# Kernel tuning notes

Measured on AMD Instinct MI355X. Metric: run time of the kernel, lower is better.

The kernel has to match this reference:

```python
import jax, jax.numpy as jnp
import numpy as np

DIM = 64
K = 7
GC = 8            # groups_channels (hardcoded in module)
G = DIM // GC     # groups = 8
RED = 2           # reduction_ratio
PAD = (K - 1) // 2


def _patches(y, k, p):
    # torch nn.Unfold(k, dilation=1, padding=p, stride=1) ordering: (c, kh, kw)
    b, c, H, W = y.shape
    yp = jnp.pad(y, ((0, 0), (0, 0), (p, p), (p, p)))
    tiles = [yp[:, :, i:i + H, j:j + W] for i in range(k) for j in range(k)]
    return jnp.stack(tiles, axis=2)  # (b, c, k*k, H, W)


def setup_inputs() -> dict:
    key = jax.random.key(0)
    ks = jax.random.split(key, 6)
    b, h, w = 4, 128, 128
    input_x = jax.random.normal(ks[0], (b, DIM, h, w), dtype=jnp.float32)
    input_y = jax.random.normal(ks[1], (b, DIM, h, w), dtype=jnp.float32)
    c_mid = DIM // RED
    w1 = jax.random.normal(ks[2], (c_mid, DIM), dtype=jnp.float32) * 0.05
    b1 = jnp.zeros((c_mid,), dtype=jnp.float32)
    w2 = jax.random.normal(ks[3], (K * K * G, c_mid), dtype=jnp.float32) * 0.05
    b2 = jnp.zeros((K * K * G,), dtype=jnp.float32)
    return {"input_x": input_x, "input_y": input_y, "w1": w1, "b1": b1, "w2": w2, "b2": b2}


def reference(input_x, input_y, w1, b1, w2, b2):
    b, c, h, w = input_x.shape
    # 1x1 convs generating dynamic kernels (stride == 1, no avgpool)
    mid = jnp.einsum('bchw,oc->bohw', input_x, w1) + b1[None, :, None, None]
    weight = jnp.einsum('bchw,oc->bohw', mid, w2) + b2[None, :, None, None]
    # (b, G, 1, k*k, h, w) broadcast over groups_channels
    weight = weight.reshape(b, G, K * K, h, w)[:, :, None]
    # unfold input_y -> (b, G, GC, k*k, h, w)
    out = _patches(input_y, K, PAD).reshape(b, G, GC, K * K, h, w)
    out = (weight * out).sum(axis=3).reshape(b, DIM, h, w)
    return out
```

## Files before the change

### kernel.cpp

```cpp
#include <hip/hip_runtime.h>
#include <hip/hip_fp16.h>

#define DIMC 64
#define KS 7
#define NTAP 49
#define GCH 8
#define NG 8
#define CMID 32
#define PADD 3
#define HH 128
#define WW 128
#define PLANE (HH*WW)
#define TW 32
#define TH 8
#define TPX (TW+2*PADD)
#define TPY (TH+2*PADD)
#define NPIX (TPX*TPY)
#define NB 4
#define WTSTR 36
#define CPAD 12

#define WC_OFF 0
#define BC_OFF 65536
#define WS_NEED ((size_t)BC_OFF + 2048)

typedef __attribute__((ext_vector_type(8))) short short8;
typedef __attribute__((ext_vector_type(4))) float f32x4;
typedef __fp16 fp16x2 __attribute__((ext_vector_type(2)));

static __device__ inline unsigned short f2bs(float f) {
    union { float f; unsigned u; } v; v.f = f;
    unsigned r = v.u + 0x7fff + ((v.u >> 16) & 1);
    return (unsigned short)(r >> 16);
}

static __device__ inline unsigned pkh(float a, float b) {
    union { fp16x2 h; unsigned u; } c;
    c.h = __builtin_amdgcn_cvt_pkrtz(a, b);
    return c.u;
}

__global__ __launch_bounds__(256)
void prep_wc(const float* __restrict__ w1, const float* __restrict__ b1,
             const float* __restrict__ w2, const float* __restrict__ b2,
             unsigned short* __restrict__ wc, float* __restrict__ bc) {
    const int idx = blockIdx.x * 256 + threadIdx.x;
    const int row64 = idx >> 4;
    const int c0 = (idx & 15) * 4;
    const int g = row64 >> 6, r = row64 & 63;
    float a0 = 0.f, a1 = 0.f, a2 = 0.f, a3 = 0.f, bv = 0.f;
    if (r < NTAP) {
        const float* w2r = w2 + (g * NTAP + r) * CMID;
        #pragma unroll
        for (int m = 0; m < CMID; ++m) {
            float wv = w2r[m];
            const float* w1r = w1 + m * DIMC + c0;
            a0 = fmaf(wv, w1r[0], a0);
            a1 = fmaf(wv, w1r[1], a1);
            a2 = fmaf(wv, w1r[2], a2);
            a3 = fmaf(wv, w1r[3], a3);
        }
        if (c0 == 0) {
            bv = b2[g * NTAP + r];
            #pragma unroll
            for (int m = 0; m < CMID; ++m) bv = fmaf(w2r[m], b1[m], bv);
        }
    }
    *reinterpret_cast<uint2*>(wc + row64 * DIMC + c0) =
        make_uint2(((unsigned)f2bs(a1) << 16) | f2bs(a0),
                   ((unsigned)f2bs(a3) << 16) | f2bs(a2));
    if ((idx & 15) == 0) bc[row64] = bv;
}

__global__ __launch_bounds__(256, 4)
void invol_mfma9_kernel(const float* __restrict__ x, const float* __restrict__ y,
                        const unsigned short* __restrict__ wc,
                        const float* __restrict__ bc,
                        float* __restrict__ out) {
    __shared__ __half ytile[NPIX * GCH];
    __shared__ __half wtl[256 * WTSTR];

    const int tid = threadIdx.x;
    const int l = tid & 63, w = tid >> 6;
    const int fr = l & 15, fk = l >> 4;
    const int bx = blockIdx.x, by = blockIdx.y;
    const int b = blockIdx.z >> 3, g = blockIdx.z & 7;
    const int tx = tid & 31, ty = tid >> 5;

    int gpix[4];
    #pragma unroll
    for (int nt = 0; nt < 4; ++nt) {
        int lp = w * 64 + nt * 16 + fr;
        gpix[nt] = (by * TH + (lp >> 5)) * WW + bx * TW + (lp & 31);
    }

    const float* xb = x + (size_t)b * DIMC * PLANE;
    short8 bf[2][4];
    #pragma unroll
    for (int kp = 0; kp < 2; ++kp)
        #pragma unroll
        for (int nt = 0; nt < 4; ++nt) {
            const float* xp = xb + (size_t)(kp * 32 + fk * 8) * PLANE + gpix[nt];
            unsigned d[4];
            #pragma unroll
            for (int jj = 0; jj < 4; ++jj) {
                float v0 = xp[(size_t)(2 * jj) * PLANE];
                float v1 = xp[(size_t)(2 * jj + 1) * PLANE];
                d[jj] = ((unsigned)f2bs(v1) << 16) | f2bs(v0);
            }
            union { uint4 u; short8 s; } cv;
            cv.u = make_uint4(d[0], d[1], d[2], d[3]);
            bf[kp][nt] = cv.s;
        }

    short8 af[4][2];
    #pragma unroll
    for (int dmt = 0; dmt < 4; ++dmt)
        #pragma unroll
        for (int kp = 0; kp < 2; ++kp) {
            union { uint4 u; short8 s; } cv;
            cv.u = *reinterpret_cast<const uint4*>(
                wc + ((size_t)(g * 64 + dmt * 16 + fr)) * DIMC + kp * 32 + fk * 8);
            af[dmt][kp] = cv.s;
        }

    const float* yg = y + (size_t)(b * DIMC + g * GCH) * PLANE;
    #pragma unroll
    for (int k = 0; k < 5; ++k) {
        int i = tid + k * 256;
        if (i < NPIX * 2) {
            int q  = i / NPIX;
            int px = i - q * NPIX;
            int r = px / TPX, col = px - r * TPX;
            int sy = by * TH + r - PADD, sx = bx * TW + col - PADD;
            bool ok = (sy >= 0 && sy < HH && sx >= 0 && sx < WW);
            const float* yp = yg + (size_t)(q * 4) * PLANE + sy * WW + sx;
            float v0 = ok ? yp[0] : 0.f;
            float v1 = ok ? yp[PLANE] : 0.f;
            float v2 = ok ? yp[2 * PLANE] : 0.f;
            float v3 = ok ? yp[3 * PLANE] : 0.f;
            *reinterpret_cast<uint2*>(&ytile[px * GCH + q * 4]) =
                make_uint2(pkh(v0, v1), pkh(v2, v3));
        }
    }

    __syncthreads();

    __half2 acch[4];
    #pragma unroll
    for (int cc = 0; cc < 4; ++cc) acch[cc] = __float2half2_rn(0.f);
    const int ybase = (ty * TPX + tx) * GCH;

    #pragma unroll
    for (int mc = 0; mc < 2; ++mc) {
        f32x4 acc[2][4];
        #pragma unroll
        for (int dm = 0; dm < 2; ++dm)
            #pragma unroll
            for (int nt = 0; nt < 4; ++nt)
                acc[dm][nt] = f32x4{0.f, 0.f, 0.f, 0.f};

        #pragma unroll
        for (int dm = 0; dm < 2; ++dm)
            #pragma unroll
            for (int kp = 0; kp < 2; ++kp)
                #pragma unroll
                for (int nt = 0; nt < 4; ++nt)
                    acc[dm][nt] = __builtin_amdgcn_mfma_f32_16x16x32_bf16(
                        af[mc * 2 + dm][kp], bf[kp][nt], acc[dm][nt], 0, 0, 0);

        #pragma unroll
        for (int dm = 0; dm < 2; ++dm) {
            int rb = (mc * 2 + dm) * 16 + fk * 4;
            float4 bb = *reinterpret_cast<const float4*>(&bc[g * 64 + rb]);
            #pragma unroll
            for (int nt = 0; nt < 4; ++nt) {
                int lp = w * 64 + nt * 16 + fr;
                *reinterpret_cast<uint2*>(&wtl[lp * WTSTR + dm * 16 + fk * 4]) =
                    make_uint2(pkh(acc[dm][nt][0] + bb.x, acc[dm][nt][1] + bb.y),
                               pkh(acc[dm][nt][2] + bb.z, acc[dm][nt][3] + bb.w));
            }
        }

        uint2 wr[8];
        #pragma unroll
        for (int q = 0; q < 8; ++q)
            wr[q] = *reinterpret_cast<const uint2*>(&wtl[tid * WTSTR + q * 4]);

        const int ninv = (mc == 0) ? 32 : 17;
        #pragma unroll
        for (int j = 0; j < 32; ++j) {
            if (j >= ninv) break;
            const int kk = mc * 32 + j;
            const int ky = kk / 7, kx = kk - ky * 7;
            unsigned uh = (j & 2) ? wr[j >> 2].y : wr[j >> 2].x;
            union { unsigned u; __half2 h; } hc; hc.u = uh;
            __half wh = (j & 1) ? __high2half(hc.h) : __low2half(hc.h);
            __half2 wv2 = __half2half2(wh);
            union { uint4 u; __half2 h[4]; } yvv;
            yvv.u = *reinterpret_cast<const uint4*>(&ytile[ybase + (ky * TPX + kx) * GCH]);
            acch[0] = __hfma2(wv2, yvv.h[0], acch[0]);
            acch[1] = __hfma2(wv2, yvv.h[1], acch[1]);
            acch[2] = __hfma2(wv2, yvv.h[2], acch[2]);
            acch[3] = __hfma2(wv2, yvv.h[3], acch[3]);
        }
    }

    const int gy = by * TH + ty, gx = bx * TW + tx;
    float* op = out + ((size_t)(b * DIMC + g * GCH) * HH + gy) * WW + gx;
    #pragma unroll
    for (int cc = 0; cc < 4; ++cc) {
        float2 f = __half22float2(acch[cc]);
        op[(2 * cc) * PLANE]     = f.x;
        op[(2 * cc + 1) * PLANE] = f.y;
    }
}

__global__ __launch_bounds__(256, 1)
void invol_fused_kernel(const float* __restrict__ x, const float* __restrict__ y,
                        const float* __restrict__ w1, const float* __restrict__ b1,
                        const float* __restrict__ w2, const float* __restrict__ b2,
                        float* __restrict__ out) {
    __shared__ float ytile[NPIX * CPAD];
    const int tid = threadIdx.x;
    const int tx = tid & 31, ty = tid >> 5;
    const int bx = blockIdx.x, by = blockIdx.y, bz = blockIdx.z;
    const int gx = bx * TW + tx, gy = by * TH + ty;

    float xv[DIMC];
    const float* xp = x + ((size_t)(bz * DIMC) * HH + gy) * WW + gx;
    #pragma unroll
    for (int c = 0; c < DIMC; ++c) xv[c] = xp[c * PLANE];

    float mid[CMID];
    #pragma unroll
    for (int m = 0; m < CMID; ++m) {
        float a = b1[m];
        const float4* w1r = reinterpret_cast<const float4*>(w1 + m * DIMC);
        #pragma unroll
        for (int cq = 0; cq < DIMC / 4; ++cq) {
            float4 wv = w1r[cq];
            a = fmaf(wv.x, xv[4*cq+0], a);
            a = fmaf(wv.y, xv[4*cq+1], a);
            a = fmaf(wv.z, xv[4*cq+2], a);
            a = fmaf(wv.w, xv[4*cq+3], a);
        }
        mid[m] = a;
    }

    for (int g = 0; g < NG; ++g) {
        __syncthreads();
        for (int i = tid; i < NPIX * GCH; i += 256) {
            int c = i / NPIX;
            int p = i - c * NPIX;
            int r = p / TPX;
            int col = p - r * TPX;
            int sy = by * TH + r - PADD;
            int sx = bx * TW + col - PADD;
            float v = 0.f;
            if (sy >= 0 && sy < HH && sx >= 0 && sx < WW)
                v = y[((size_t)(bz * DIMC + g * GCH + c) * HH + sy) * WW + sx];
            ytile[p * CPAD + c] = v;
        }
        __syncthreads();

        float wt[NTAP];
        const float*  b2g = b2 + g * NTAP;
        const float4* w2g = reinterpret_cast<const float4*>(w2 + g * NTAP * CMID);
        #pragma unroll
        for (int kk = 0; kk < NTAP; ++kk) {
            float a = b2g[kk];
            #pragma unroll
            for (int mq = 0; mq < CMID / 4; ++mq) {
                float4 wv = w2g[kk * (CMID / 4) + mq];
                a = fmaf(wv.x, mid[4*mq+0], a);
                a = fmaf(wv.y, mid[4*mq+1], a);
                a = fmaf(wv.z, mid[4*mq+2], a);
                a = fmaf(wv.w, mid[4*mq+3], a);
            }
            wt[kk] = a;
        }

        float acc[GCH];
        #pragma unroll
        for (int cc = 0; cc < GCH; ++cc) acc[cc] = 0.f;
        #pragma unroll
        for (int ky = 0; ky < KS; ++ky) {
            #pragma unroll
            for (int kx = 0; kx < KS; ++kx) {
                float wv = wt[ky * KS + kx];
                int pp = (ty + ky) * TPX + (tx + kx);
                const float4* yr = reinterpret_cast<const float4*>(&ytile[pp * CPAD]);
                float4 ya = yr[0];
                float4 yb = yr[1];
                acc[0] = fmaf(wv, ya.x, acc[0]);
                acc[1] = fmaf(wv, ya.y, acc[1]);
                acc[2] = fmaf(wv, ya.z, acc[2]);
                acc[3] = fmaf(wv, ya.w, acc[3]);
                acc[4] = fmaf(wv, yb.x, acc[4]);
                acc[5] = fmaf(wv, yb.y, acc[5]);
                acc[6] = fmaf(wv, yb.z, acc[6]);
                acc[7] = fmaf(wv, yb.w, acc[7]);
            }
        }

        float* op = out + ((size_t)(bz * DIMC + g * GCH) * HH + gy) * WW + gx;
        #pragma unroll
        for (int cc = 0; cc < GCH; ++cc) op[cc * PLANE] = acc[cc];
    }
}

extern "C" void kernel_launch(void* const* d_in, const int* in_sizes, int n_in,
                              void* d_out, int out_size, void* d_ws, size_t ws_size,
                              hipStream_t stream) {
    const float* x  = (const float*)d_in[0];
    const float* y  = (const float*)d_in[1];
    const float* w1 = (const float*)d_in[2];
    const float* b1 = (const float*)d_in[3];
    const float* w2 = (const float*)d_in[4];
    const float* b2 = (const float*)d_in[5];
    float* out = (float*)d_out;

    if (ws_size >= WS_NEED) {
        char* ws = (char*)d_ws;
        unsigned short* wcp = (unsigned short*)(ws + WC_OFF);
        float*          bcp = (float*)(ws + BC_OFF);

        hipLaunchKernelGGL(prep_wc, dim3(32), dim3(256), 0, stream,
                           w1, b1, w2, b2, wcp, bcp);
        hipLaunchKernelGGL(invol_mfma9_kernel, dim3(WW / TW, HH / TH, NB * NG), dim3(256), 0, stream,
                           x, y, wcp, bcp, out);
    } else {
        dim3 grid(WW / TW, HH / TH, NB);
        hipLaunchKernelGGL(invol_fused_kernel, grid, dim3(256), 0, stream,
                           x, y, w1, b1, w2, b2, out);
    }
}
```

Measured before the change: 36.55 us.

## Pre-convert x to channel-interleaved bf16 layout in prep kernel

Adds a pre-pass inside the prep kernel that converts x into a bf16 layout with 8 channels per pixel packed contiguously, stored in workspace. The main kernel then loads each MFMA B fragment with one 16-byte vector load instead of 8 strided fp32 loads plus conversions. Before this, each of the 8 group blocks per batch re-read and re-converted all of x, so the conversion is now done once. The cost is an extra 8 MB workspace write and read, and a larger workspace requirement that could trigger the fallback path if the workspace is too small.

After: 34.54 us. 5.5% less time.

```diff
diff --git a/kernel.cpp b/kernel.cpp
--- a/kernel.cpp
+++ b/kernel.cpp
@@ -22,7 +22,8 @@
 
 #define WC_OFF 0
 #define BC_OFF 65536
-#define WS_NEED ((size_t)BC_OFF + 2048)
+#define XT_OFF 67584
+#define WS_NEED ((size_t)XT_OFF + 8388608)
 
 typedef __attribute__((ext_vector_type(8))) short short8;
 typedef __attribute__((ext_vector_type(4))) float f32x4;
@@ -41,42 +42,65 @@
 }
 
 __global__ __launch_bounds__(256)
-void prep_wc(const float* __restrict__ w1, const float* __restrict__ b1,
-             const float* __restrict__ w2, const float* __restrict__ b2,
-             unsigned short* __restrict__ wc, float* __restrict__ bc) {
-    const int idx = blockIdx.x * 256 + threadIdx.x;
-    const int row64 = idx >> 4;
-    const int c0 = (idx & 15) * 4;
-    const int g = row64 >> 6, r = row64 & 63;
-    float a0 = 0.f, a1 = 0.f, a2 = 0.f, a3 = 0.f, bv = 0.f;
-    if (r < NTAP) {
-        const float* w2r = w2 + (g * NTAP + r) * CMID;
-        #pragma unroll
-        for (int m = 0; m < CMID; ++m) {
-            float wv = w2r[m];
-            const float* w1r = w1 + m * DIMC + c0;
-            a0 = fmaf(wv, w1r[0], a0);
-            a1 = fmaf(wv, w1r[1], a1);
-            a2 = fmaf(wv, w1r[2], a2);
-            a3 = fmaf(wv, w1r[3], a3);
-        }
-        if (c0 == 0) {
-            bv = b2[g * NTAP + r];
-            #pragma unroll
-            for (int m = 0; m < CMID; ++m) bv = fmaf(w2r[m], b1[m], bv);
-        }
-    }
-    *reinterpret_cast<uint2*>(wc + row64 * DIMC + c0) =
-        make_uint2(((unsigned)f2bs(a1) << 16) | f2bs(a0),
-                   ((unsigned)f2bs(a3) << 16) | f2bs(a2));
-    if ((idx & 15) == 0) bc[row64] = bv;
+void prep_all(const float* __restrict__ x,
+              const float* __restrict__ w1, const float* __restrict__ b1,
+              const float* __restrict__ w2, const float* __restrict__ b2,
+              unsigned short* __restrict__ wc, float* __restrict__ bc,
+              unsigned short* __restrict__ xt) {
+    const int bid = blockIdx.x;
+    if (bid < 512) {
+        const int pxblk = bid & 63, rest = bid >> 6;
+        const int b = rest & 3, h = rest >> 2;
+        const int px = pxblk * 256 + threadIdx.x;
+        const float* xp = x + (size_t)b * DIMC * PLANE + (size_t)h * 32 * PLANE + px;
+        #pragma unroll
+        for (int q = 0; q < 4; ++q) {
+            unsigned pk[4];
+            #pragma unroll
+            for (int j = 0; j < 4; ++j) {
+                float v0 = xp[(size_t)(q * 8 + 2 * j) * PLANE];
+                float v1 = xp[(size_t)(q * 8 + 2 * j + 1) * PLANE];
+                pk[j] = ((unsigned)f2bs(v1) << 16) | f2bs(v0);
+            }
+            *reinterpret_cast<uint4*>(xt + (((size_t)b * 8 + h * 4 + q) * PLANE + px) * 8) =
+                make_uint4(pk[0], pk[1], pk[2], pk[3]);
+        }
+    } else {
+        const int idx = (bid - 512) * 256 + threadIdx.x;
+        const int row64 = idx >> 4;
+        const int c0 = (idx & 15) * 4;
+        const int g = row64 >> 6, r = row64 & 63;
+        float a0 = 0.f, a1 = 0.f, a2 = 0.f, a3 = 0.f, bv = 0.f;
+        if (r < NTAP) {
+            const float* w2r = w2 + (g * NTAP + r) * CMID;
+            #pragma unroll
+            for (int m = 0; m < CMID; ++m) {
+                float wv = w2r[m];
+                const float* w1r = w1 + m * DIMC + c0;
+                a0 = fmaf(wv, w1r[0], a0);
+                a1 = fmaf(wv, w1r[1], a1);
+                a2 = fmaf(wv, w1r[2], a2);
+                a3 = fmaf(wv, w1r[3], a3);
+            }
+            if (c0 == 0) {
+                bv = b2[g * NTAP + r];
+                #pragma unroll
+                for (int m = 0; m < CMID; ++m) bv = fmaf(w2r[m], b1[m], bv);
+            }
+        }
+        *reinterpret_cast<uint2*>(wc + row64 * DIMC + c0) =
+            make_uint2(((unsigned)f2bs(a1) << 16) | f2bs(a0),
+                       ((unsigned)f2bs(a3) << 16) | f2bs(a2));
+        if ((idx & 15) == 0) bc[row64] = bv;
+    }
 }
 
 __global__ __launch_bounds__(256, 4)
-void invol_mfma9_kernel(const float* __restrict__ x, const float* __restrict__ y,
-                        const unsigned short* __restrict__ wc,
-                        const float* __restrict__ bc,
-                        float* __restrict__ out) {
+void invol_mfma10_kernel(const float* __restrict__ y,
+                         const unsigned short* __restrict__ xt,
+                         const unsigned short* __restrict__ wc,
+                         const float* __restrict__ bc,
+                         float* __restrict__ out) {
     __shared__ __half ytile[NPIX * GCH];
     __shared__ __half wtl[256 * WTSTR];
 
@@ -93,26 +117,16 @@
         int lp = w * 64 + nt * 16 + fr;
         gpix[nt] = (by * TH + (lp >> 5)) * WW + bx * TW + (lp & 31);
     }
-
-    const float* xb = x + (size_t)b * DIMC * PLANE;
     short8 bf[2][4];
     #pragma unroll
     for (int kp = 0; kp < 2; ++kp)
         #pragma unroll
         for (int nt = 0; nt < 4; ++nt) {
-            const float* xp = xb + (size_t)(kp * 32 + fk * 8) * PLANE + gpix[nt];
-            unsigned d[4];
-            #pragma unroll
-            for (int jj = 0; jj < 4; ++jj) {
-                float v0 = xp[(size_t)(2 * jj) * PLANE];
-                float v1 = xp[(size_t)(2 * jj + 1) * PLANE];
-                d[jj] = ((unsigned)f2bs(v1) << 16) | f2bs(v0);
-            }
             union { uint4 u; short8 s; } cv;
-            cv.u = make_uint4(d[0], d[1], d[2], d[3]);
+            cv.u = *reinterpret_cast<const uint4*>(
+                xt + (((size_t)b * 8 + kp * 4 + fk) * PLANE + gpix[nt]) * 8);
             bf[kp][nt] = cv.s;
         }
-
     short8 af[4][2];
     #pragma unroll
     for (int dmt = 0; dmt < 4; ++dmt)
@@ -325,11 +339,12 @@
         char* ws = (char*)d_ws;
         unsigned short* wcp = (unsigned short*)(ws + WC_OFF);
         float*          bcp = (float*)(ws + BC_OFF);
-
-        hipLaunchKernelGGL(prep_wc, dim3(32), dim3(256), 0, stream,
-                           w1, b1, w2, b2, wcp, bcp);
-        hipLaunchKernelGGL(invol_mfma9_kernel, dim3(WW / TW, HH / TH, NB * NG), dim3(256), 0, stream,
-                           x, y, wcp, bcp, out);
+        unsigned short* xtp = (unsigned short*)(ws + XT_OFF);
+
+        hipLaunchKernelGGL(prep_all, dim3(512 + 32), dim3(256), 0, stream,
+                           x, w1, b1, w2, b2, wcp, bcp, xtp);
+        hipLaunchKernelGGL(invol_mfma10_kernel, dim3(WW / TW, HH / TH, NB * NG), dim3(256), 0, stream,
+                           y, xtp, wcp, bcp, out);
     } else {
         dim3 grid(WW / TW, HH / TH, NB);
         hipLaunchKernelGGL(invol_fused_kernel, grid, dim3(256), 0, stream,
```
